# Optimization experiments

Hardware: AMD Instinct MI355X
Metric: run time of the kernel (lower is better)

Reference implementation:

```python
import jax, jax.numpy as jnp
import numpy as np
import math

N_HEAD = 16
ROPE_BASE = 10000.0


def _rope(xh):
    # xh: [B, H, T, D]; rotate full head dim using half-split (GPT-NeoX style)
    B, H, T, D = xh.shape
    theta = 1.0 / (ROPE_BASE ** (jnp.arange(0, D, 2, dtype=jnp.float32) / D))  # [D/2]
    idx_theta = jnp.arange(T, dtype=jnp.float32)[:, None] * theta[None, :]      # [T, D/2]
    idx_theta2 = jnp.concatenate([idx_theta, idx_theta], axis=1)                 # [T, D]
    cos = jnp.cos(idx_theta2)[None, None]                                        # [1,1,T,D]
    sin = jnp.sin(idx_theta2)[None, None]
    d2 = D // 2
    neg_half = jnp.concatenate([-xh[..., d2:], xh[..., :d2]], axis=-1)
    return xh * cos + neg_half * sin


def setup_inputs() -> dict:
    key = jax.random.key(0)
    k1, k2, k3 = jax.random.split(key, 3)
    B, T, C = 2, 2048, 2048
    x = jax.random.normal(k1, (B, T, C), dtype=jnp.float32)
    w_attn = jax.random.normal(k2, (C, 3 * C), dtype=jnp.float32) * (1.0 / math.sqrt(C))
    w_proj = jax.random.normal(k3, (C, C), dtype=jnp.float32) * (1.0 / math.sqrt(C))
    return {"x": x, "w_attn": w_attn, "w_proj": w_proj}


def reference(x, w_attn, w_proj):
    B, T, C = x.shape
    H = N_HEAD
    D = C // H
    qkv = x @ w_attn                                   # [B,T,3C]
    q, k, v = jnp.split(qkv, 3, axis=-1)
    # [B,T,C] -> [B,H,T,D]
    to_heads = lambda t: t.reshape(B, T, H, D).transpose(0, 2, 1, 3)
    q, k, v = to_heads(q), to_heads(k), to_heads(v)
    q = _rope(q)
    k = _rope(k)
    att = jnp.einsum('bhqd,bhkd->bhqk', q, k) * (1.0 / math.sqrt(D))
    causal = jnp.tril(jnp.ones((T, T), dtype=bool))
    att = jnp.where(causal[None, None], att, -jnp.inf)
    att = jax.nn.softmax(att, axis=-1)
    y = jnp.einsum('bhqk,bhkd->bhqd', att, v)          # [B,H,T,D]
    y = y.transpose(0, 2, 1, 3).reshape(B, T, C)
    return y @ w_proj
```

## Files before the change

kernel.cpp:

```cpp
#include <hip/hip_runtime.h>
#include <hip/hip_bf16.h>
#include <math.h>

typedef __bf16 bf16;
typedef __bf16 bf16x8 __attribute__((ext_vector_type(8)));
typedef __bf16 bf16x4v __attribute__((ext_vector_type(4)));
typedef float f32x4 __attribute__((ext_vector_type(4)));
typedef float f32x16 __attribute__((ext_vector_type(16)));
typedef unsigned int u32x2 __attribute__((ext_vector_type(2)));
typedef unsigned int u32x4 __attribute__((ext_vector_type(4)));

#define MFMA16(a, b, c) __builtin_amdgcn_mfma_f32_16x16x32_bf16((a), (b), (c), 0, 0, 0)
#define MFMA32(a, b, c) __builtin_amdgcn_mfma_f32_32x32x16_bf16((a), (b), (c), 0, 0, 0)

static constexpr int Bsz = 2, Tsz = 2048, Csz = 2048, Hn = 16, Dh = 128;
static constexpr float ATTN_SCALE = 0.08838834764831845f;

__device__ __forceinline__ void gld16(const void* src, void* dst) {
    __builtin_amdgcn_global_load_lds((__attribute__((address_space(1))) void*)src,
                                     (__attribute__((address_space(3))) void*)dst,
                                     16, 0, 0);
}

__device__ __forceinline__ unsigned cvt_pk_bf16(float lo, float hi) {
    unsigned r;
    asm("v_cvt_pk_bf16_f32 %0, %1, %2" : "=v"(r) : "v"(lo), "v"(hi));
    return r;
}

__device__ __forceinline__ bf16x8 make_pfrag(float p0, float p1, float p2, float p3,
                                             float p4, float p5, float p6, float p7) {
    unsigned a0 = cvt_pk_bf16(p0, p1), a1 = cvt_pk_bf16(p2, p3);
    unsigned b0 = cvt_pk_bf16(p4, p5), b1 = cvt_pk_bf16(p6, p7);
    asm volatile("v_permlane32_swap_b32 %0, %1" : "+v"(a0), "+v"(b0));
    asm volatile("v_permlane32_swap_b32 %0, %1" : "+v"(a1), "+v"(b1));
    u32x4 w = {a0, a1, b0, b1};
    return __builtin_bit_cast(bf16x8, w);
}

__global__ __launch_bounds__(256) void cast_x_kernel(const float* __restrict__ x,
                                                     bf16* __restrict__ o, int n8) {
    int i = blockIdx.x * 256 + threadIdx.x;
    if (i >= n8) return;
    const float4* x4 = (const float4*)x;
    float4 a = x4[2 * i], b = x4[2 * i + 1];
    bf16x8 v;
    v[0] = (bf16)a.x; v[1] = (bf16)a.y; v[2] = (bf16)a.z; v[3] = (bf16)a.w;
    v[4] = (bf16)b.x; v[5] = (bf16)b.y; v[6] = (bf16)b.z; v[7] = (bf16)b.w;
    ((bf16x8*)o)[i] = v;
}

template <typename TIN>
__global__ __launch_bounds__(256) void transpose_cast_kernel(const TIN* __restrict__ in,
                                                             bf16* __restrict__ out,
                                                             int R, int Cc) {
    __shared__ float tile[64][65];
    const int tx = threadIdx.x, ty = threadIdx.y;
    in  += (size_t)blockIdx.z * R * Cc;
    out += (size_t)blockIdx.z * R * Cc;
    const int c0 = blockIdx.x * 64, r0 = blockIdx.y * 64;
#pragma unroll
    for (int j = 0; j < 16; ++j) {
        int rr = ty + j * 4;
        tile[rr][tx] = (float)in[(size_t)(r0 + rr) * Cc + c0 + tx];
    }
    __syncthreads();
    const int q = (tx & 15) << 2;
    const int cg = tx >> 4;
#pragma unroll
    for (int j = 0; j < 4; ++j) {
        const int cc = j * 16 + cg * 4 + ty;
        bf16x4v v;
        v[0] = (bf16)tile[q + 0][cc];
        v[1] = (bf16)tile[q + 1][cc];
        v[2] = (bf16)tile[q + 2][cc];
        v[3] = (bf16)tile[q + 3][cc];
        *(bf16x4v*)(out + (size_t)(c0 + cc) * R + r0 + q) = v;
    }
}

__global__ __launch_bounds__(256) void cossin_kernel(float2* __restrict__ cs) {
    int idx = blockIdx.x * 256 + threadIdx.x;
    int t = idx >> 6, i = idx & 63;
    float theta = 1.0f / powf(10000.0f, (float)(2 * i) / 128.0f);
    float ang = (float)t * theta;
    cs[idx] = make_float2(cosf(ang), sinf(ang));
}

__global__ __launch_bounds__(512, 2)
void gemm384_qkv(const bf16* __restrict__ A, const bf16* __restrict__ Bt,
                 bf16* __restrict__ Oq, bf16* __restrict__ Ok, bf16* __restrict__ Vt,
                 const float2* __restrict__ cs, int K) {
    __shared__ bf16 sA[2][128 * 64];
    __shared__ bf16 sB[2][384 * 64];
    const int tid = threadIdx.x, lane = tid & 63, wid = tid >> 6;
    const int wm = wid >> 2, wn = wid & 3;
    const int lo16 = lane & 15, hi4 = lane >> 4;

    const int cpx = gridDim.x >> 3;
    const int swz = (blockIdx.x & 7) * cpx + (blockIdx.x >> 3);
    const int by = swz & 31;
    const int bx = swz >> 5;
    const int row0 = by << 7, col0 = bx * 384;

    const int srow = tid >> 3;
    const int swzoff = (((tid & 7) ^ ((tid >> 3) & 7)) << 3);
    const bf16* srcA = A  + (size_t)(row0 + srow) * K + swzoff;
    const bf16* srcB = Bt + (size_t)(col0 + srow) * K + swzoff;
    const size_t K64 = (size_t)K * 64;
    char* const ldsA = (char*)&sA[0][0];
    char* const ldsB = (char*)&sB[0][0];
    const int wuo = wid << 10;

    auto issueA = [&](int c, int kt) {
        const bf16* s = srcA + (size_t)kt * 64;
        gld16(s,       ldsA + c * 16384 + 0    + wuo);
        gld16(s + K64, ldsA + c * 16384 + 8192 + wuo);
    };
    auto issueB = [&](int c, int kt, int u) {
        const bf16* s = srcB + (size_t)kt * 64 + (size_t)(2 * u) * K64;
        gld16(s,       ldsB + c * 49152 + u * 16384 + 0    + wuo);
        gld16(s + K64, ldsB + c * 49152 + u * 16384 + 8192 + wuo);
    };
    auto ldF = [&](const char* buf, int row, int ks) {
        return *(const bf16x8*)(buf + row * 128 + ((((ks << 2) + hi4) ^ (row & 7)) << 4));
    };

    const int arow = (wm << 6) + lo16;
    const int brow = (wn << 4) + lo16;

    f32x4 acc[4][6] = {};
    const int nkt = K >> 6;

    issueA(0, 0); issueB(0, 0, 0); issueB(0, 0, 1); issueB(0, 0, 2);
    asm volatile("s_waitcnt vmcnt(4)" ::: "memory");
    __builtin_amdgcn_s_barrier();

    for (int kt = 0; kt < nkt - 1; ++kt) {
        const int c = kt & 1;
        const char* bufA = ldsA + c * 16384;
        const char* bufB = ldsB + c * 49152;
        bf16x8 af[4][2], bq[2][2];
#pragma unroll
        for (int i = 0; i < 4; ++i) {
            af[i][0] = ldF(bufA, arow + (i << 4), 0);
            af[i][1] = ldF(bufA, arow + (i << 4), 1);
        }
#pragma unroll
        for (int j = 0; j < 2; ++j) {
            bq[j][0] = ldF(bufB, brow + (j << 6), 0);
            bq[j][1] = ldF(bufB, brow + (j << 6), 1);
        }
        issueA(c ^ 1, kt + 1); issueB(c ^ 1, kt + 1, 0); issueB(c ^ 1, kt + 1, 1);
        __builtin_amdgcn_s_barrier();
        asm volatile("s_waitcnt lgkmcnt(0)" ::: "memory");
        __builtin_amdgcn_sched_barrier(0);
        __builtin_amdgcn_s_setprio(1);
#pragma unroll
        for (int ks = 0; ks < 2; ++ks)
#pragma unroll
            for (int i = 0; i < 4; ++i)
#pragma unroll
                for (int j = 0; j < 2; ++j)
                    acc[i][j] = MFMA16(af[i][ks], bq[j][ks], acc[i][j]);
        __builtin_amdgcn_s_setprio(0);
        asm volatile("s_waitcnt vmcnt(8)" ::: "memory");
        __builtin_amdgcn_s_barrier();
#pragma unroll
        for (int j = 0; j < 2; ++j) {
            bq[j][0] = ldF(bufB, brow + ((j + 2) << 6), 0);
            bq[j][1] = ldF(bufB, brow + ((j + 2) << 6), 1);
        }
        issueB(c ^ 1, kt + 1, 2);
        __builtin_amdgcn_s_barrier();
        asm volatile("s_waitcnt lgkmcnt(0)" ::: "memory");
        __builtin_amdgcn_sched_barrier(0);
        __builtin_amdgcn_s_setprio(1);
#pragma unroll
        for (int ks = 0; ks < 2; ++ks)
#pragma unroll
            for (int i = 0; i < 4; ++i)
#pragma unroll
                for (int j = 0; j < 2; ++j)
                    acc[i][j + 2] = MFMA16(af[i][ks], bq[j][ks], acc[i][j + 2]);
        __builtin_amdgcn_s_setprio(0);
        asm volatile("s_waitcnt vmcnt(8)" ::: "memory");
        __builtin_amdgcn_s_barrier();
#pragma unroll
        for (int j = 0; j < 2; ++j) {
            bq[j][0] = ldF(bufB, brow + ((j + 4) << 6), 0);
            bq[j][1] = ldF(bufB, brow + ((j + 4) << 6), 1);
        }
        __builtin_amdgcn_s_barrier();
        asm volatile("s_waitcnt lgkmcnt(0)" ::: "memory");
        __builtin_amdgcn_sched_barrier(0);
        __builtin_amdgcn_s_setprio(1);
#pragma unroll
        for (int ks = 0; ks < 2; ++ks)
#pragma unroll
            for (int i = 0; i < 4; ++i)
#pragma unroll
                for (int j = 0; j < 2; ++j)
                    acc[i][j + 4] = MFMA16(af[i][ks], bq[j][ks], acc[i][j + 4]);
        __builtin_amdgcn_s_setprio(0);
        asm volatile("s_waitcnt vmcnt(4)" ::: "memory");
        __builtin_amdgcn_s_barrier();
    }

    {
        const int c = (nkt - 1) & 1;
        const char* bufA = ldsA + c * 16384;
        const char* bufB = ldsB + c * 49152;
        bf16x8 af[4][2], bq[2][2];
#pragma unroll
        for (int i = 0; i < 4; ++i) {
            af[i][0] = ldF(bufA, arow + (i << 4), 0);
            af[i][1] = ldF(bufA, arow + (i << 4), 1);
        }
#pragma unroll
        for (int j = 0; j < 2; ++j) {
            bq[j][0] = ldF(bufB, brow + (j << 6), 0);
            bq[j][1] = ldF(bufB, brow + (j << 6), 1);
        }
        __builtin_amdgcn_s_barrier();
        asm volatile("s_waitcnt lgkmcnt(0)" ::: "memory");
        __builtin_amdgcn_sched_barrier(0);
        __builtin_amdgcn_s_setprio(1);
#pragma unroll
        for (int ks = 0; ks < 2; ++ks)
#pragma unroll
            for (int i = 0; i < 4; ++i)
#pragma unroll
                for (int j = 0; j < 2; ++j)
                    acc[i][j] = MFMA16(af[i][ks], bq[j][ks], acc[i][j]);
        __builtin_amdgcn_s_setprio(0);
        asm volatile("s_waitcnt vmcnt(2)" ::: "memory");
        __builtin_amdgcn_s_barrier();
#pragma unroll
        for (int j = 0; j < 2; ++j) {
            bq[j][0] = ldF(bufB, brow + ((j + 2) << 6), 0);
            bq[j][1] = ldF(bufB, brow + ((j + 2) << 6), 1);
        }
        __builtin_amdgcn_s_barrier();
        asm volatile("s_waitcnt lgkmcnt(0)" ::: "memory");
        __builtin_amdgcn_sched_barrier(0);
        __builtin_amdgcn_s_setprio(1);
#pragma unroll
        for (int ks = 0; ks < 2; ++ks)
#pragma unroll
            for (int i = 0; i < 4; ++i)
#pragma unroll
                for (int j = 0; j < 2; ++j)
                    acc[i][j + 2] = MFMA16(af[i][ks], bq[j][ks], acc[i][j + 2]);
        __builtin_amdgcn_s_setprio(0);
        asm volatile("s_waitcnt vmcnt(0)" ::: "memory");
        __builtin_amdgcn_s_barrier();
#pragma unroll
        for (int j = 0; j < 2; ++j) {
            bq[j][0] = ldF(bufB, brow + ((j + 4) << 6), 0);
            bq[j][1] = ldF(bufB, brow + ((j + 4) << 6), 1);
        }
        __builtin_amdgcn_s_barrier();
        asm volatile("s_waitcnt lgkmcnt(0)" ::: "memory");
        __builtin_amdgcn_sched_barrier(0);
        __builtin_amdgcn_s_setprio(1);
#pragma unroll
        for (int ks = 0; ks < 2; ++ks)
#pragma unroll
            for (int i = 0; i < 4; ++i)
#pragma unroll
                for (int j = 0; j < 2; ++j)
                    acc[i][j + 4] = MFMA16(af[i][ks], bq[j][ks], acc[i][j + 4]);
        __builtin_amdgcn_s_setprio(0);
    }

    const int d = (wn << 4) + lo16;
#pragma unroll
    for (int p = 0; p < 3; ++p) {
        const int gcb = col0 + (p << 7);
        const int seg = gcb >> 11;
        const int hb = (gcb >> 7) & 15;
        if (seg < 2) {
            bf16* dst0 = (seg == 0) ? Oq : Ok;
            const float qs = (seg == 0) ? ATTN_SCALE : 1.0f;
#pragma unroll
            for (int mi = 0; mi < 4; ++mi)
#pragma unroll
                for (int r = 0; r < 4; ++r) {
                    const int gm = row0 + (wm << 6) + (mi << 4) + (hi4 << 2) + r;
                    const int b = gm >> 11, t = gm & 2047;
                    const float2 csv = cs[t * 64 + d];
                    bf16* drow = dst0 + ((((size_t)b * Hn + hb) * Tsz + t) << 7);
                    const float vlo = acc[mi][2 * p][r];
                    const float vhi = acc[mi][2 * p + 1][r];
                    drow[d]      = (bf16)((vlo * csv.x - vhi * csv.y) * qs);
                    drow[d + 64] = (bf16)((vhi * csv.x + vlo * csv.y) * qs);
                }
        } else {
#pragma unroll
            for (int mi = 0; mi < 4; ++mi) {
                const int t0 = row0 + (wm << 6) + (mi << 4) + (hi4 << 2);
                const int b = t0 >> 11, tt = t0 & 2047;
                bf16* vbase = Vt + (((size_t)b * Hn + hb) * Dh) * Tsz + tt;
                u32x2 wlo = {cvt_pk_bf16(acc[mi][2 * p][0], acc[mi][2 * p][1]),
                             cvt_pk_bf16(acc[mi][2 * p][2], acc[mi][2 * p][3])};
                u32x2 whi = {cvt_pk_bf16(acc[mi][2 * p + 1][0], acc[mi][2 * p + 1][1]),
                             cvt_pk_bf16(acc[mi][2 * p + 1][2], acc[mi][2 * p + 1][3])};
                *(u32x2*)(vbase + (size_t)d * Tsz)        = wlo;
                *(u32x2*)(vbase + (size_t)(d + 64) * Tsz) = whi;
            }
        }
    }
}

__global__ __launch_bounds__(512, 2)
void gemm256_proj(const bf16* __restrict__ A, const bf16* __restrict__ Bt,
                  float* __restrict__ Cf, int K) {
    __shared__ bf16 sA[2][128 * 64];
    __shared__ bf16 sB[2][256 * 64];
    const int tid = threadIdx.x, lane = tid & 63, wid = tid >> 6;
    const int wm = wid >> 2, wn = wid & 3;
    const int lo16 = lane & 15, hi4 = lane >> 4;
    const int N = 2048;

    const int cpx = gridDim.x >> 3;
    const int swz = (blockIdx.x & 7) * cpx + (blockIdx.x >> 3);
    const int by = swz & 31;
    const int bx = swz >> 5;
    const int row0 = by << 7, col0 = bx << 8;

    const int srow = tid >> 3;
    const int swzoff = (((tid & 7) ^ ((tid >> 3) & 7)) << 3);
    const bf16* srcA = A  + (size_t)(row0 + srow) * K + swzoff;
    const bf16* srcB = Bt + (size_t)(col0 + srow) * K + swzoff;
    const size_t K64 = (size_t)K * 64;
    char* const ldsA = (char*)&sA[0][0];
    char* const ldsB = (char*)&sB[0][0];
    const int wuo = wid << 10;

    auto issueA = [&](int c, int kt) {
        const bf16* s = srcA + (size_t)kt * 64;
        gld16(s,       ldsA + c * 16384 + 0    + wuo);
        gld16(s + K64, ldsA + c * 16384 + 8192 + wuo);
    };
    auto issueB = [&](int c, int kt, int u) {
        const bf16* s = srcB + (size_t)kt * 64 + (size_t)(2 * u) * K64;
        gld16(s,       ldsB + c * 32768 + u * 16384 + 0    + wuo);
        gld16(s + K64, ldsB + c * 32768 + u * 16384 + 8192 + wuo);
    };
    auto ldF = [&](const char* buf, int row, int ks) {
        return *(const bf16x8*)(buf + row * 128 + ((((ks << 2) + hi4) ^ (row & 7)) << 4));
    };

    const int arow = (wm << 6) + lo16;
    const int brow = (wn << 4) + lo16;

    f32x4 acc[4][4] = {};
    const int nkt = K >> 6;

    issueA(0, 0); issueB(0, 0, 0); issueB(0, 0, 1);
    if (nkt > 1) { issueA(1, 1); issueB(1, 1, 0); }
    asm volatile("s_waitcnt vmcnt(4)" ::: "memory");
    __builtin_amdgcn_s_barrier();

    for (int kt = 0; kt < nkt; ++kt) {
        const int c = kt & 1;
        const char* bufA = ldsA + c * 16384;
        const char* bufB = ldsB + c * 32768;
        bf16x8 af[4][2], bq[2][2];
#pragma unroll
        for (int i = 0; i < 4; ++i) {
            af[i][0] = ldF(bufA, arow + (i << 4), 0);
            af[i][1] = ldF(bufA, arow + (i << 4), 1);
        }
#pragma unroll
        for (int j = 0; j < 2; ++j) {
            bq[j][0] = ldF(bufB, brow + (j << 6), 0);
            bq[j][1] = ldF(bufB, brow + (j << 6), 1);
        }
        if (kt + 1 < nkt) issueB(c ^ 1, kt + 1, 1);
        __builtin_amdgcn_s_barrier();
        asm volatile("s_waitcnt lgkmcnt(0)" ::: "memory");
        __builtin_amdgcn_sched_barrier(0);
        __builtin_amdgcn_s_setprio(1);
#pragma unroll
        for (int ks = 0; ks < 2; ++ks)
#pragma unroll
            for (int i = 0; i < 4; ++i)
#pragma unroll
                for (int j = 0; j < 2; ++j)
                    acc[i][j] = MFMA16(af[i][ks], bq[j][ks], acc[i][j]);
        __builtin_amdgcn_s_setprio(0);
        if (kt + 1 < nkt) asm volatile("s_waitcnt vmcnt(6)" ::: "memory");
        else              asm volatile("s_waitcnt vmcnt(0)" ::: "memory");
        __builtin_amdgcn_s_barrier();
#pragma unroll
        for (int j = 0; j < 2; ++j) {
            bq[j][0] = ldF(bufB, brow + ((j + 2) << 6), 0);
            bq[j][1] = ldF(bufB, brow + ((j + 2) << 6), 1);
        }
        if (kt + 2 < nkt) { issueA(c, kt + 2); issueB(c, kt + 2, 0); }
        __builtin_amdgcn_s_barrier();
        asm volatile("s_waitcnt lgkmcnt(0)" ::: "memory");
        __builtin_amdgcn_sched_barrier(0);
        __builtin_amdgcn_s_setprio(1);
#pragma unroll
        for (int ks = 0; ks < 2; ++ks)
#pragma unroll
            for (int i = 0; i < 4; ++i)
#pragma unroll
                for (int j = 0; j < 2; ++j)
                    acc[i][j + 2] = MFMA16(af[i][ks], bq[j][ks], acc[i][j + 2]);
        __builtin_amdgcn_s_setprio(0);
        if (kt + 2 < nkt)      asm volatile("s_waitcnt vmcnt(6)" ::: "memory");
        else if (kt + 1 < nkt) asm volatile("s_waitcnt vmcnt(2)" ::: "memory");
        __builtin_amdgcn_s_barrier();
    }

#pragma unroll
    for (int mi = 0; mi < 4; ++mi)
#pragma unroll
        for (int r = 0; r < 4; ++r) {
            const int gm = row0 + (wm << 6) + (mi << 4) + (hi4 << 2) + r;
            float* crow = Cf + (size_t)gm * N + col0 + (wn << 4) + lo16;
#pragma unroll
            for (int nj = 0; nj < 4; ++nj)
                crow[nj << 6] = acc[mi][nj][r];
        }
}

__device__ __forceinline__ void stage_tile(const bf16* __restrict__ Kb,
                                           const bf16* __restrict__ Vtb,
                                           bf16* sKc, bf16* sVc, int k0, int tid) {
#pragma unroll
    for (int c = 0; c < 4; ++c) {
        const int off = (c << 12) + (tid << 4);
        const int row = off >> 8, u = (off >> 4) & 15;
        gld16(Kb + (size_t)(k0 + row) * Dh + ((u ^ (row & 7)) << 3), (char*)sKc + off);
        const int dv = off >> 7, uv = (off >> 4) & 7;
        gld16(Vtb + (size_t)dv * Tsz + k0 + ((uv ^ (dv & 7)) << 3), (char*)sVc + off);
    }
}

__global__ __launch_bounds__(256, 2)
void attn_kernel(const bf16* __restrict__ Q, const bf16* __restrict__ K,
                 const bf16* __restrict__ Vt, bf16* __restrict__ Y) {
    __shared__ bf16 sK[2][64 * 128];
    __shared__ bf16 sV[2][128 * 64];
    const int tid = threadIdx.x, lane = tid & 63, wv = tid >> 6;
    const int lo32 = lane & 31, hl = lane >> 5;

    const int i = blockIdx.x;
    const int g = i >> 5;
    const int bh = i & 31;
    const int t = (i < 256) ? (15 - g) : (g - 8);
    const int b = bh >> 4, h = bh & 15;

    const int q0 = t << 7;
    const int q0w = q0 + (wv << 5);
    const int qg = q0w + lo32;

    const bf16* Kb  = K  + (size_t)bh * (Tsz * Dh);
    const bf16* Vtb = Vt + (size_t)bh * (Tsz * Dh);
    const bf16* Qp  = Q  + (size_t)bh * (Tsz * Dh) + (size_t)qg * Dh;

    bf16x8 qf[8];
#pragma unroll
    for (int kc = 0; kc < 8; ++kc)
        qf[kc] = *(const bf16x8*)(Qp + (kc << 4) + (hl << 3));

    float m = -1e30f, lsum = 0.f;
    f32x16 o[4] = {};

    const int nt_block = 2 * t + 2;
    const int nt_warp = ((q0w + 31) >> 6) + 1;

    stage_tile(Kb, Vtb, &sK[0][0], &sV[0][0], 0, tid);

    int cur = 0;
    for (int kt = 0; kt < nt_block; ++kt) {
        __syncthreads();
        if (kt + 1 < nt_block)
            stage_tile(Kb, Vtb, &sK[cur ^ 1][0], &sV[cur ^ 1][0], (kt + 1) << 6, tid);
        if (kt < nt_warp) {
            const int k0 = kt << 6;
            const bf16* kbuf = &sK[cur][0];
            const bf16* vbuf = &sV[cur][0];
            f32x16 s0 = {}, s1 = {};
            const int swk = lo32 & 7;
            __builtin_amdgcn_s_setprio(1);
#pragma unroll
            for (int kc = 0; kc < 8; ++kc) {
                bf16x8 kf0 = *(const bf16x8*)((const char*)kbuf + lo32 * 256 +
                              ((((kc << 1) + hl) ^ swk) << 4));
                s0 = MFMA32(kf0, qf[kc], s0);
                bf16x8 kf1 = *(const bf16x8*)((const char*)kbuf + (32 + lo32) * 256 +
                              ((((kc << 1) + hl) ^ swk) << 4));
                s1 = MFMA32(kf1, qf[kc], s1);
            }
            __builtin_amdgcn_s_setprio(0);

            const bool bnd = (k0 + 63 > q0w);
            if (bnd) {
#pragma unroll
                for (int r = 0; r < 16; ++r) {
                    const int kl = (r & 3) + ((r >> 2) << 3) + (hl << 2);
                    if (k0 + kl > qg)      s0[r] = -1e30f;
                    if (k0 + 32 + kl > qg) s1[r] = -1e30f;
                }
            }
            float pm = s0[0];
#pragma unroll
            for (int r = 1; r < 16; ++r) pm = fmaxf(pm, s0[r]);
#pragma unroll
            for (int r = 0; r < 16; ++r) pm = fmaxf(pm, s1[r]);
            pm = fmaxf(pm, __shfl_xor(pm, 32));

            if (__any(pm > m + 8.0f)) {
                const float mn = fmaxf(m, pm);
                const float sc = __expf(m - mn);
                m = mn;
                lsum *= sc;
#pragma unroll
                for (int db = 0; db < 4; ++db)
#pragma unroll
                    for (int r = 0; r < 16; ++r) o[db][r] *= sc;
            }
            float rs = 0.f;
            if (bnd) {
#pragma unroll
                for (int r = 0; r < 16; ++r) {
                    float e0 = (s0[r] > -1e29f) ? __expf(s0[r] - m) : 0.f;
                    float e1 = (s1[r] > -1e29f) ? __expf(s1[r] - m) : 0.f;
                    s0[r] = e0; s1[r] = e1; rs += e0 + e1;
                }
            } else {
#pragma unroll
                for (int r = 0; r < 16; ++r) {
                    float e0 = __expf(s0[r] - m);
                    float e1 = __expf(s1[r] - m);
                    s0[r] = e0; s1[r] = e1; rs += e0 + e1;
                }
            }
            rs += __shfl_xor(rs, 32);
            lsum += rs;

            bf16x8 pb0 = make_pfrag(s0[0], s0[1], s0[2],  s0[3],  s0[4],  s0[5],  s0[6],  s0[7]);
            bf16x8 pb1 = make_pfrag(s0[8], s0[9], s0[10], s0[11], s0[12], s0[13], s0[14], s0[15]);
            bf16x8 pb2 = make_pfrag(s1[0], s1[1], s1[2],  s1[3],  s1[4],  s1[5],  s1[6],  s1[7]);
            bf16x8 pb3 = make_pfrag(s1[8], s1[9], s1[10], s1[11], s1[12], s1[13], s1[14], s1[15]);

            __builtin_amdgcn_s_setprio(1);
#pragma unroll
            for (int db = 0; db < 4; ++db) {
                const int rd = (db << 5) + lo32;
                const char* vrow = (const char*)vbuf + rd * 128;
                const int sw = rd & 7;
                bf16x8 v0 = *(const bf16x8*)(vrow + (((0 + hl) ^ sw) << 4));
                o[db] = MFMA32(v0, pb0, o[db]);
                bf16x8 v1 = *(const bf16x8*)(vrow + (((2 + hl) ^ sw) << 4));
                o[db] = MFMA32(v1, pb1, o[db]);
                bf16x8 v2 = *(const bf16x8*)(vrow + (((4 + hl) ^ sw) << 4));
                o[db] = MFMA32(v2, pb2, o[db]);
                bf16x8 v3 = *(const bf16x8*)(vrow + (((6 + hl) ^ sw) << 4));
                o[db] = MFMA32(v3, pb3, o[db]);
            }
            __builtin_amdgcn_s_setprio(0);
        }
        cur ^= 1;
    }

    const float inv = 1.0f / lsum;
    const size_t rowoff = ((size_t)b * Tsz + qg) * (size_t)Csz + (size_t)h * 128;
#pragma unroll
    for (int db = 0; db < 4; ++db)
#pragma unroll
        for (int gg = 0; gg < 4; ++gg) {
            unsigned w0 = cvt_pk_bf16(o[db][4 * gg + 0] * inv, o[db][4 * gg + 1] * inv);
            unsigned w1 = cvt_pk_bf16(o[db][4 * gg + 2] * inv, o[db][4 * gg + 3] * inv);
            u32x2 w = {w0, w1};
            *(u32x2*)(Y + rowoff + (db << 5) + (gg << 3) + (hl << 2)) = w;
        }
}

extern "C" void kernel_launch(void* const* d_in, const int* in_sizes, int n_in,
                              void* d_out, int out_size, void* d_ws, size_t ws_size,
                              hipStream_t stream) {
    const float* x      = (const float*)d_in[0];
    const float* w_attn = (const float*)d_in[1];
    const float* w_proj = (const float*)d_in[2];
    float* out = (float*)d_out;

    char* ws = (char*)d_ws;
    bf16* Xb  = (bf16*)(ws);
    bf16* Wat = (bf16*)(ws + 16777216);
    bf16* Wpt = (bf16*)(ws + 41943040);
    bf16* Qr  = (bf16*)(ws + 50331648);
    bf16* Kr  = (bf16*)(ws + 67108864);
    bf16* Vt  = (bf16*)(ws + 100663296);
    bf16* Yb  = (bf16*)(ws + 117440512);
    float2* cs = (float2*)(ws + 134217728);

    cast_x_kernel<<<4096, 256, 0, stream>>>(x, Xb, (Bsz * Tsz * Csz) / 8);
    transpose_cast_kernel<float><<<dim3(96, 32, 1), dim3(64, 4), 0, stream>>>(w_attn, Wat, 2048, 6144);
    transpose_cast_kernel<float><<<dim3(32, 32, 1), dim3(64, 4), 0, stream>>>(w_proj, Wpt, 2048, 2048);
    cossin_kernel<<<512, 256, 0, stream>>>(cs);

    gemm384_qkv<<<512, 512, 0, stream>>>(Xb, Wat, Qr, Kr, Vt, cs, 2048);

    attn_kernel<<<dim3(512), 256, 0, stream>>>(Qr, Kr, Vt, Yb);

    gemm256_proj<<<256, 512, 0, stream>>>(Yb, Wpt, out, 2048);
}
```

Baseline: 235.0 us.

## Pair high and low causal query tiles per attention block sharing K/V staging

Each attention block now handles two query tiles of the same head, one near the end (t_hi) and one near the start (t_lo). Both reuse the same staged K/V tiles in shared memory, which balances the causal workload per block and halves the K/V loads for the low tile. The grid is halved to 256 blocks and launch bounds drop to one block per SM. This doubles the register state (two Q fragment sets and accumulators), which lowers occupancy, and 256 blocks may underfill a device with 256 CUs.

```diff
diff --git a/kernel.cpp b/kernel.cpp
--- a/kernel.cpp
+++ b/kernel.cpp
@@ -442,7 +442,93 @@
     }
 }
 
-__global__ __launch_bounds__(256, 2)
+__device__ __forceinline__ void attn_tile(const bf16* kbuf, const bf16* vbuf,
+                                          const bf16x8* qf, int k0, int q0w, int qg,
+                                          int lo32, int hl,
+                                          float& m, float& lsum, f32x16* o) {
+    f32x16 s0 = {}, s1 = {};
+    const int swk = lo32 & 7;
+    __builtin_amdgcn_s_setprio(1);
+#pragma unroll
+    for (int kc = 0; kc < 8; ++kc) {
+        bf16x8 kf0 = *(const bf16x8*)((const char*)kbuf + lo32 * 256 +
+                      ((((kc << 1) + hl) ^ swk) << 4));
+        s0 = MFMA32(kf0, qf[kc], s0);
+        bf16x8 kf1 = *(const bf16x8*)((const char*)kbuf + (32 + lo32) * 256 +
+                      ((((kc << 1) + hl) ^ swk) << 4));
+        s1 = MFMA32(kf1, qf[kc], s1);
+    }
+    __builtin_amdgcn_s_setprio(0);
+
+    const bool bnd = (k0 + 63 > q0w);
+    if (bnd) {
+#pragma unroll
+        for (int r = 0; r < 16; ++r) {
+            const int kl = (r & 3) + ((r >> 2) << 3) + (hl << 2);
+            if (k0 + kl > qg)      s0[r] = -1e30f;
+            if (k0 + 32 + kl > qg) s1[r] = -1e30f;
+        }
+    }
+    float pm = s0[0];
+#pragma unroll
+    for (int r = 1; r < 16; ++r) pm = fmaxf(pm, s0[r]);
+#pragma unroll
+    for (int r = 0; r < 16; ++r) pm = fmaxf(pm, s1[r]);
+    pm = fmaxf(pm, __shfl_xor(pm, 32));
+
+    if (__any(pm > m + 8.0f)) {
+        const float mn = fmaxf(m, pm);
+        const float sc = __expf(m - mn);
+        m = mn;
+        lsum *= sc;
+#pragma unroll
+        for (int db = 0; db < 4; ++db)
+#pragma unroll
+            for (int r = 0; r < 16; ++r) o[db][r] *= sc;
+    }
+    float rs = 0.f;
+    if (bnd) {
+#pragma unroll
+        for (int r = 0; r < 16; ++r) {
+            float e0 = (s0[r] > -1e29f) ? __expf(s0[r] - m) : 0.f;
+            float e1 = (s1[r] > -1e29f) ? __expf(s1[r] - m) : 0.f;
+            s0[r] = e0; s1[r] = e1; rs += e0 + e1;
+        }
+    } else {
+#pragma unroll
+        for (int r = 0; r < 16; ++r) {
+            float e0 = __expf(s0[r] - m);
+            float e1 = __expf(s1[r] - m);
+            s0[r] = e0; s1[r] = e1; rs += e0 + e1;
+        }
+    }
+    rs += __shfl_xor(rs, 32);
+    lsum += rs;
+
+    bf16x8 pb0 = make_pfrag(s0[0], s0[1], s0[2],  s0[3],  s0[4],  s0[5],  s0[6],  s0[7]);
+    bf16x8 pb1 = make_pfrag(s0[8], s0[9], s0[10], s0[11], s0[12], s0[13], s0[14], s0[15]);
+    bf16x8 pb2 = make_pfrag(s1[0], s1[1], s1[2],  s1[3],  s1[4],  s1[5],  s1[6],  s1[7]);
+    bf16x8 pb3 = make_pfrag(s1[8], s1[9], s1[10], s1[11], s1[12], s1[13], s1[14], s1[15]);
+
+    __builtin_amdgcn_s_setprio(1);
+#pragma unroll
+    for (int db = 0; db < 4; ++db) {
+        const int rd = (db << 5) + lo32;
+        const char* vrow = (const char*)vbuf + rd * 128;
+        const int sw = rd & 7;
+        bf16x8 v0 = *(const bf16x8*)(vrow + (((0 + hl) ^ sw) << 4));
+        o[db] = MFMA32(v0, pb0, o[db]);
+        bf16x8 v1 = *(const bf16x8*)(vrow + (((2 + hl) ^ sw) << 4));
+        o[db] = MFMA32(v1, pb1, o[db]);
+        bf16x8 v2 = *(const bf16x8*)(vrow + (((4 + hl) ^ sw) << 4));
+        o[db] = MFMA32(v2, pb2, o[db]);
+        bf16x8 v3 = *(const bf16x8*)(vrow + (((6 + hl) ^ sw) << 4));
+        o[db] = MFMA32(v3, pb3, o[db]);
+    }
+    __builtin_amdgcn_s_setprio(0);
+}
+
+__global__ __launch_bounds__(256, 1)
 void attn_kernel(const bf16* __restrict__ Q, const bf16* __restrict__ K,
                  const bf16* __restrict__ Vt, bf16* __restrict__ Y) {
     __shared__ bf16 sK[2][64 * 128];
@@ -451,136 +537,74 @@
     const int lo32 = lane & 31, hl = lane >> 5;
 
     const int i = blockIdx.x;
-    const int g = i >> 5;
-    const int bh = i & 31;
-    const int t = (i < 256) ? (15 - g) : (g - 8);
+    const int slot = i >> 3;
+    const int bh = ((i & 7) << 2) + (slot & 3);
+    const int p = slot >> 2;
+    const int t_hi = 15 - p, t_lo = p;
     const int b = bh >> 4, h = bh & 15;
-
-    const int q0 = t << 7;
-    const int q0w = q0 + (wv << 5);
-    const int qg = q0w + lo32;
 
     const bf16* Kb  = K  + (size_t)bh * (Tsz * Dh);
     const bf16* Vtb = Vt + (size_t)bh * (Tsz * Dh);
-    const bf16* Qp  = Q  + (size_t)bh * (Tsz * Dh) + (size_t)qg * Dh;
-
-    bf16x8 qf[8];
-#pragma unroll
-    for (int kc = 0; kc < 8; ++kc)
-        qf[kc] = *(const bf16x8*)(Qp + (kc << 4) + (hl << 3));
-
-    float m = -1e30f, lsum = 0.f;
-    f32x16 o[4] = {};
-
-    const int nt_block = 2 * t + 2;
-    const int nt_warp = ((q0w + 31) >> 6) + 1;
+    const bf16* Qbh = Q  + (size_t)bh * (Tsz * Dh);
+
+    const int q0w_hi = (t_hi << 7) + (wv << 5), qg_hi = q0w_hi + lo32;
+    const int q0w_lo = (t_lo << 7) + (wv << 5), qg_lo = q0w_lo + lo32;
+
+    bf16x8 qfh[8], qfl[8];
+#pragma unroll
+    for (int kc = 0; kc < 8; ++kc) {
+        qfh[kc] = *(const bf16x8*)(Qbh + (size_t)qg_hi * Dh + (kc << 4) + (hl << 3));
+        qfl[kc] = *(const bf16x8*)(Qbh + (size_t)qg_lo * Dh + (kc << 4) + (hl << 3));
+    }
+
+    float mh = -1e30f, lh = 0.f, ml = -1e30f, ll = 0.f;
+    f32x16 oh[4] = {}, ol[4] = {};
+
+    const int nt = 2 * t_hi + 2;
+    const int nth = ((q0w_hi + 31) >> 6) + 1;
+    const int ntl = ((q0w_lo + 31) >> 6) + 1;
 
     stage_tile(Kb, Vtb, &sK[0][0], &sV[0][0], 0, tid);
 
     int cur = 0;
-    for (int kt = 0; kt < nt_block; ++kt) {
+    for (int kt = 0; kt < nt; ++kt) {
         __syncthreads();
-        if (kt + 1 < nt_block)
+        if (kt + 1 < nt)
             stage_tile(Kb, Vtb, &sK[cur ^ 1][0], &sV[cur ^ 1][0], (kt + 1) << 6, tid);
-        if (kt < nt_warp) {
-            const int k0 = kt << 6;
-            const bf16* kbuf = &sK[cur][0];
-            const bf16* vbuf = &sV[cur][0];
-            f32x16 s0 = {}, s1 = {};
-            const int swk = lo32 & 7;
-            __builtin_amdgcn_s_setprio(1);
-#pragma unroll
-            for (int kc = 0; kc < 8; ++kc) {
-                bf16x8 kf0 = *(const bf16x8*)((const char*)kbuf + lo32 * 256 +
-                              ((((kc << 1) + hl) ^ swk) << 4));
-                s0 = MFMA32(kf0, qf[kc], s0);
-                bf16x8 kf1 = *(const bf16x8*)((const char*)kbuf + (32 + lo32) * 256 +
-                              ((((kc << 1) + hl) ^ swk) << 4));
-                s1 = MFMA32(kf1, qf[kc], s1);
+        const bf16* kbuf = &sK[cur][0];
+        const bf16* vbuf = &sV[cur][0];
+        const int k0 = kt << 6;
+        if (kt < nth) attn_tile(kbuf, vbuf, qfh, k0, q0w_hi, qg_hi, lo32, hl, mh, lh, oh);
+        if (kt < ntl) attn_tile(kbuf, vbuf, qfl, k0, q0w_lo, qg_lo, lo32, hl, ml, ll, ol);
+        cur ^= 1;
+    }
+
+    {
+        const float inv = 1.0f / lh;
+        const size_t rowoff = ((size_t)b * Tsz + qg_hi) * (size_t)Csz + (size_t)h * 128;
+#pragma unroll
+        for (int db = 0; db < 4; ++db)
+#pragma unroll
+            for (int gg = 0; gg < 4; ++gg) {
+                unsigned w0 = cvt_pk_bf16(oh[db][4 * gg + 0] * inv, oh[db][4 * gg + 1] * inv);
+                unsigned w1 = cvt_pk_bf16(oh[db][4 * gg + 2] * inv, oh[db][4 * gg + 3] * inv);
+                u32x2 w = {w0, w1};
+                *(u32x2*)(Y + rowoff + (db << 5) + (gg << 3) + (hl << 2)) = w;
             }
-            __builtin_amdgcn_s_setprio(0);
-
-            const bool bnd = (k0 + 63 > q0w);
-            if (bnd) {
-#pragma unroll
-                for (int r = 0; r < 16; ++r) {
-                    const int kl = (r & 3) + ((r >> 2) << 3) + (hl << 2);
-                    if (k0 + kl > qg)      s0[r] = -1e30f;
-                    if (k0 + 32 + kl > qg) s1[r] = -1e30f;
-                }
+    }
+    {
+        const float inv = 1.0f / ll;
+        const size_t rowoff = ((size_t)b * Tsz + qg_lo) * (size_t)Csz + (size_t)h * 128;
+#pragma unroll
+        for (int db = 0; db < 4; ++db)
+#pragma unroll
+            for (int gg = 0; gg < 4; ++gg) {
+                unsigned w0 = cvt_pk_bf16(ol[db][4 * gg + 0] * inv, ol[db][4 * gg + 1] * inv);
+                unsigned w1 = cvt_pk_bf16(ol[db][4 * gg + 2] * inv, ol[db][4 * gg + 3] * inv);
+                u32x2 w = {w0, w1};
+                *(u32x2*)(Y + rowoff + (db << 5) + (gg << 3) + (hl << 2)) = w;
             }
-            float pm = s0[0];
-#pragma unroll
-            for (int r = 1; r < 16; ++r) pm = fmaxf(pm, s0[r]);
-#pragma unroll
-            for (int r = 0; r < 16; ++r) pm = fmaxf(pm, s1[r]);
-            pm = fmaxf(pm, __shfl_xor(pm, 32));
-
-            if (__any(pm > m + 8.0f)) {
-                const float mn = fmaxf(m, pm);
-                const float sc = __expf(m - mn);
-                m = mn;
-                lsum *= sc;
-#pragma unroll
-                for (int db = 0; db < 4; ++db)
-#pragma unroll
-                    for (int r = 0; r < 16; ++r) o[db][r] *= sc;
-            }
-            float rs = 0.f;
-            if (bnd) {
-#pragma unroll
-                for (int r = 0; r < 16; ++r) {
-                    float e0 = (s0[r] > -1e29f) ? __expf(s0[r] - m) : 0.f;
-                    float e1 = (s1[r] > -1e29f) ? __expf(s1[r] - m) : 0.f;
-                    s0[r] = e0; s1[r] = e1; rs += e0 + e1;
-                }
-            } else {
-#pragma unroll
-                for (int r = 0; r < 16; ++r) {
-                    float e0 = __expf(s0[r] - m);
-                    float e1 = __expf(s1[r] - m);
-                    s0[r] = e0; s1[r] = e1; rs += e0 + e1;
-                }
-            }
-            rs += __shfl_xor(rs, 32);
-            lsum += rs;
-
-            bf16x8 pb0 = make_pfrag(s0[0], s0[1], s0[2],  s0[3],  s0[4],  s0[5],  s0[6],  s0[7]);
-            bf16x8 pb1 = make_pfrag(s0[8], s0[9], s0[10], s0[11], s0[12], s0[13], s0[14], s0[15]);
-            bf16x8 pb2 = make_pfrag(s1[0], s1[1], s1[2],  s1[3],  s1[4],  s1[5],  s1[6],  s1[7]);
-            bf16x8 pb3 = make_pfrag(s1[8], s1[9], s1[10], s1[11], s1[12], s1[13], s1[14], s1[15]);
-
-            __builtin_amdgcn_s_setprio(1);
-#pragma unroll
-            for (int db = 0; db < 4; ++db) {
-                const int rd = (db << 5) + lo32;
-                const char* vrow = (const char*)vbuf + rd * 128;
-                const int sw = rd & 7;
-                bf16x8 v0 = *(const bf16x8*)(vrow + (((0 + hl) ^ sw) << 4));
-                o[db] = MFMA32(v0, pb0, o[db]);
-                bf16x8 v1 = *(const bf16x8*)(vrow + (((2 + hl) ^ sw) << 4));
-                o[db] = MFMA32(v1, pb1, o[db]);
-                bf16x8 v2 = *(const bf16x8*)(vrow + (((4 + hl) ^ sw) << 4));
-                o[db] = MFMA32(v2, pb2, o[db]);
-                bf16x8 v3 = *(const bf16x8*)(vrow + (((6 + hl) ^ sw) << 4));
-                o[db] = MFMA32(v3, pb3, o[db]);
-            }
-            __builtin_amdgcn_s_setprio(0);
-        }
-        cur ^= 1;
-    }
-
-    const float inv = 1.0f / lsum;
-    const size_t rowoff = ((size_t)b * Tsz + qg) * (size_t)Csz + (size_t)h * 128;
-#pragma unroll
-    for (int db = 0; db < 4; ++db)
-#pragma unroll
-        for (int gg = 0; gg < 4; ++gg) {
-            unsigned w0 = cvt_pk_bf16(o[db][4 * gg + 0] * inv, o[db][4 * gg + 1] * inv);
-            unsigned w1 = cvt_pk_bf16(o[db][4 * gg + 2] * inv, o[db][4 * gg + 3] * inv);
-            u32x2 w = {w0, w1};
-            *(u32x2*)(Y + rowoff + (db << 5) + (gg << 3) + (hl << 2)) = w;
-        }
+    }
 }
 
 extern "C" void kernel_launch(void* const* d_in, const int* in_sizes, int n_in,
@@ -608,7 +632,7 @@
 
     gemm384_qkv<<<512, 512, 0, stream>>>(Xb, Wat, Qr, Kr, Vt, cs, 2048);
 
-    attn_kernel<<<dim3(512), 256, 0, stream>>>(Qr, Kr, Vt, Yb);
+    attn_kernel<<<dim3(256), 256, 0, stream>>>(Qr, Kr, Vt, Yb);
 
     gemm256_proj<<<256, 512, 0, stream>>>(Yb, Wpt, out, 2048);
 }
```

New measurement: 252.4 us. +7.4%, slower.
